# Performance work log

Hardware: AMD Instinct MI355X
Metric: run time of the kernel (lower is better)

Reference implementation:

```python
import jax, jax.numpy as jnp
import numpy as np
jax.config.update("jax_enable_x64", True)

N = 16384   # nodes
C = 16      # initial color vocabulary size
B = 64      # number of graphs in the batch
_rs = np.random.RandomState(42)
_MULTS = jnp.asarray((_rs.randint(1, 2 ** 62, size=C + 1).astype(np.int64) << 1) | 1)  # odd 64-bit hash multipliers


def setup_inputs() -> dict:
    key = jax.random.key(0)
    k1, k2, k3 = jax.random.split(key, 3)
    x = jax.random.randint(k1, (N,), 0, C, dtype=jnp.int64)
    adj_t = jax.random.randint(k2, (N, N), 0, 2).astype(jnp.float32)  # dense binary adjacency
    batch = jnp.sort(jax.random.randint(k3, (N,), 0, B, dtype=jnp.int64))
    return {"x": x, "adj_t": adj_t, "batch": batch}


def _wl_colors(x, adj_t):
    # One WL refinement step. The torch code hashes (own_color, sorted neighbor colors)
    # and assigns new ids by insertion order into an OrderedDict ('isolate' -> 0).
    # A sorted tuple of neighbor colors is equivalent to the neighbor color multiset,
    # which we represent as a count histogram and hash with a 64-bit wraparound
    # polynomial hash; ids are then assigned by first-occurrence (node-index) order.
    n = x.shape[0]
    onehot = jax.nn.one_hot(x, C, dtype=adj_t.dtype)                 # [N, C]
    nbr_hist = jnp.round(adj_t @ onehot).astype(jnp.int64)           # [N, C] neighbor color counts
    iso = (adj_t.sum(axis=1) + adj_t.sum(axis=0)) == 0               # isolated nodes
    h = x * _MULTS[0] + (nbr_hist * _MULTS[1:]).sum(axis=-1)         # int64 wraparound hash
    h = jnp.where(iso, jnp.int64(-(2 ** 63)), h)
    order = jnp.argsort(h)
    hs = h[order]
    new_grp = jnp.concatenate([jnp.ones((1,), bool), hs[1:] != hs[:-1]])
    gid = jnp.zeros(n, jnp.int64).at[order].set(jnp.cumsum(new_grp) - 1)   # group id per node
    first_of_grp = jax.ops.segment_min(jnp.arange(n), gid, num_segments=n)
    firsts = first_of_grp[gid]                                       # first node index with same signature
    is_first = (~iso) & (firsts == jnp.arange(n))
    rank = jnp.cumsum(is_first.astype(jnp.int64))                    # hashmap insertion order (1-based)
    return jnp.where(iso, 0, rank[firsts])                           # 'isolate' -> 0


def _histogram(colors, batch):
    # Per-graph color histogram; width padded to N+1 (max possible distinct colors)
    # for static shapes -- extra columns are zero and do not affect the L2 norm.
    num_colors = N + 1
    idx = batch * num_colors + colors
    out = jnp.zeros(B * num_colors, jnp.int64).at[idx].add(1)
    out = out.reshape(B, num_colors)[:, 1:]                          # drop 'isolate' column
    out = out.astype(jnp.float64)
    return out / jnp.linalg.norm(out, axis=-1, keepdims=True)


def reference(x, adj_t, batch):
    colors = _wl_colors(x, adj_t)          # forward's default return value
    hist = _histogram(colors, batch)       # return_embedding=True output
    return hist, colors
```

## Files before the change

### kernel.cpp

```cpp
#include <hip/hip_runtime.h>
#include <stdint.h>

#define NN 16384
#define NC 16
#define NB 64

typedef unsigned int vuint4 __attribute__((ext_vector_type(4)));

struct Mults { unsigned long long m[17]; };


__global__ __launch_bounds__(256) void k_init(const int* __restrict__ x,
                                              unsigned long long* __restrict__ table,
                                              int* __restrict__ scount,
                                              int* __restrict__ cnt) {
  int idx = blockIdx.x * 256 + threadIdx.x;
  if (idx == 0) *scount = 0;
  if (idx < 4096) {
    int c = idx & 15, k = (idx >> 4) & 3, chunk = idx >> 6;
    unsigned long long m = 0ull;
    for (int l = 0; l < 64; ++l) {
      int col = chunk * 256 + l * 4 + k;
      if (x[col] == c) m |= (1ull << l);
    }
    table[idx] = m;
  }
  int4 z = {0, 0, 0, 0};
  int4* c4 = (int4*)cnt;
  #pragma unroll
  for (int r = 0; r < 4; ++r) c4[(size_t)idx * 4 + r] = z;
}

__global__ __launch_bounds__(256) void k_hist(const float* __restrict__ adj,
                                              const unsigned long long* __restrict__ table,
                                              const int* __restrict__ x,
                                              Mults M,
                                              unsigned long long* __restrict__ h,
                                              int* __restrict__ iso,
                                              int* __restrict__ firsts,
                                              int* __restrict__ suspects,
                                              int* __restrict__ scount) {
  int wave = threadIdx.x >> 6;
  int lane = threadIdx.x & 63;
  int row  = blockIdx.x * 4 + wave;
  int xv   = x[row];
  const vuint4* rowp = (const vuint4*)(adj + (size_t)row * NN);
  int c = lane & 15, k = lane >> 6 ? 0 : (lane >> 4);
  k = lane >> 4;
  const unsigned long long* tk = table + (k * 16 + c);
  int cnt = 0;
  #pragma unroll 4
  for (int chunk = 0; chunk < 64; ++chunk) {
    vuint4 v = __builtin_nontemporal_load(&rowp[chunk * 64 + lane]);
    unsigned long long tm = tk[chunk * 64];
    unsigned long long b0 = __ballot(v.x != 0u);
    unsigned long long b1 = __ballot(v.y != 0u);
    unsigned long long b2 = __ballot(v.z != 0u);
    unsigned long long b3 = __ballot(v.w != 0u);
    unsigned long long m = (k & 2) ? ((k & 1) ? b3 : b2) : ((k & 1) ? b1 : b0);
    cnt += __popcll(m & tm);
  }
  cnt += __shfl_xor(cnt, 16, 64);
  cnt += __shfl_xor(cnt, 32, 64);
  int rs = cnt;
  rs += __shfl_xor(rs, 1, 64);
  rs += __shfl_xor(rs, 2, 64);
  rs += __shfl_xor(rs, 4, 64);
  rs += __shfl_xor(rs, 8, 64);
  unsigned long long hl = (unsigned long long)(long long)cnt * M.m[(lane & 15) + 1];
  hl += __shfl_xor(hl, 1, 64);
  hl += __shfl_xor(hl, 2, 64);
  hl += __shfl_xor(hl, 4, 64);
  hl += __shfl_xor(hl, 8, 64);
  if (lane == 0) {
    h[row] = hl + (unsigned long long)(long long)xv * M.m[0];
    if (rs == 0) { int s = atomicAdd(scount, 1); suspects[s] = row; }
  }
  if (lane == 1) iso[row] = 0;
  if (lane == 2) firsts[row] = 0x7fffffff;
}

__global__ __launch_bounds__(256) void k_colcheck(const float* __restrict__ adj,
                                                  const int* __restrict__ suspects,
                                                  const int* __restrict__ scount,
                                                  int* __restrict__ iso,
                                                  unsigned long long* __restrict__ h) {
  __shared__ int red[256];
  int nsus = *scount;
  for (int u = blockIdx.x; u < nsus; u += gridDim.x) {
    int col = suspects[u];
    int any = 0;
    for (int r = threadIdx.x; r < NN; r += 256)
      any |= (adj[(size_t)r * NN + col] != 0.0f);
    red[threadIdx.x] = any;
    __syncthreads();
    for (int s = 128; s > 0; s >>= 1) {
      if (threadIdx.x < s) red[threadIdx.x] |= red[threadIdx.x + s];
      __syncthreads();
    }
    if (threadIdx.x == 0 && red[0] == 0) {
      iso[col] = 1;
      h[col] = 0x8000000000000000ull;
    }
    __syncthreads();
  }
}

#define JC 2048
__global__ __launch_bounds__(256) void k_firsts(const unsigned long long* __restrict__ h,
                                                int* __restrict__ firsts) {
  __shared__ unsigned long long hs[JC];
  int jbase = blockIdx.y * JC;
  for (int t = threadIdx.x; t < JC; t += 256) hs[t] = h[jbase + t];
  __syncthreads();
  int i = blockIdx.x * 256 + threadIdx.x;
  unsigned long long hi = h[i];
  int best = 0x7fffffff;
  #pragma unroll 8
  for (int jj = 0; jj < JC; ++jj) {
    if (hs[jj] == hi) best = min(best, jbase + jj);
  }
  if (best < 0x7fffffff) atomicMin(&firsts[i], best);
}

__global__ __launch_bounds__(1024) void k_scan(const int* __restrict__ iso,
                                               const int* __restrict__ firsts,
                                               const int* __restrict__ batch,
                                               float* __restrict__ out_colors,
                                               int* __restrict__ cnt) {
  __shared__ int rank_lds[NN];
  __shared__ int wsum[16];
  int t = threadIdx.x;
  int lane = t & 63, wv = t >> 6;
  int base = t * 16;
  int loc[16];
  int s = 0;
  #pragma unroll
  for (int u = 0; u < 16; ++u) {
    int i = base + u;
    int isf = (!iso[i]) && (firsts[i] == i);
    s += isf;
    loc[u] = s;
  }
  int incl = s;
  #pragma unroll
  for (int off = 1; off < 64; off <<= 1) {
    int v = __shfl_up(incl, off, 64);
    if (lane >= off) incl += v;
  }
  if (lane == 63) wsum[wv] = incl;
  __syncthreads();
  if (t == 0) {
    int acc = 0;
    #pragma unroll
    for (int w = 0; w < 16; ++w) { int v = wsum[w]; wsum[w] = acc; acc += v; }
  }
  __syncthreads();
  int excl = wsum[wv] + incl - s;
  #pragma unroll
  for (int u = 0; u < 16; ++u) rank_lds[base + u] = excl + loc[u];
  __syncthreads();
  #pragma unroll
  for (int u = 0; u < 16; ++u) {
    int i = base + u;
    int c = iso[i] ? 0 : rank_lds[firsts[i]];
    out_colors[i] = (float)c;
    if (c > 0) atomicAdd(&cnt[(size_t)batch[i] * NN + (c - 1)], 1);
  }
}

__global__ __launch_bounds__(256) void k_norm(const int* __restrict__ cnt,
                                              float* __restrict__ out) {
  __shared__ float red[256];
  int b = blockIdx.x;
  const int4* c4 = (const int4*)(cnt + (size_t)b * NN);
  float4* o4 = (float4*)(out + (size_t)b * NN);
  float ss = 0.0f;
  for (int j = threadIdx.x; j < NN / 4; j += 256) {
    int4 v = c4[j];
    float4 f = {(float)v.x, (float)v.y, (float)v.z, (float)v.w};
    ss += f.x * f.x + f.y * f.y + f.z * f.z + f.w * f.w;
  }
  red[threadIdx.x] = ss;
  __syncthreads();
  for (int s = 128; s > 0; s >>= 1) {
    if (threadIdx.x < s) red[threadIdx.x] += red[threadIdx.x + s];
    __syncthreads();
  }
  float inv = 1.0f / sqrtf(red[0]);
  for (int j = threadIdx.x; j < NN / 4; j += 256) {
    int4 v = c4[j];
    float4 f = {(float)v.x * inv, (float)v.y * inv, (float)v.z * inv, (float)v.w * inv};
    o4[j] = f;
  }
}


struct MTState { uint32_t mt[624]; int idx; };

static void mt_seed(MTState& s, uint32_t seed) {
  s.mt[0] = seed;
  for (int i = 1; i < 624; ++i)
    s.mt[i] = 1812433253u * (s.mt[i - 1] ^ (s.mt[i - 1] >> 30)) + (uint32_t)i;
  s.idx = 624;
}

static uint32_t mt_next(MTState& s) {
  if (s.idx >= 624) {
    for (int i = 0; i < 624; ++i) {
      uint32_t y = (s.mt[i] & 0x80000000u) | (s.mt[(i + 1) % 624] & 0x7fffffffu);
      uint32_t nx = s.mt[(i + 397) % 624] ^ (y >> 1);
      if (y & 1u) nx ^= 2567483615u;
      s.mt[i] = nx;
    }
    s.idx = 0;
  }
  uint32_t y = s.mt[s.idx++];
  y ^= y >> 11;
  y ^= (y << 7) & 2636928640u;
  y ^= (y << 15) & 4022730752u;
  y ^= y >> 18;
  return y;
}

static uint64_t mt_next64(MTState& s) {
  uint64_t hi = mt_next(s);
  uint64_t lo = mt_next(s);
  return (hi << 32) | lo;
}


extern "C" void kernel_launch(void* const* d_in, const int* in_sizes, int n_in,
                              void* d_out, int out_size, void* d_ws, size_t ws_size,
                              hipStream_t stream) {
  const int*   x     = (const int*)d_in[0];
  const float* adj   = (const float*)d_in[1];
  const int*   batch = (const int*)d_in[2];
  float* out_hist   = (float*)d_out;
  float* out_colors = out_hist + (size_t)NB * NN;

  char* ws = (char*)d_ws;
  int*                cnt      = (int*)(ws + 0);
  int*                scount   = (int*)(ws + 4194304);
  int*                suspects = (int*)(ws + 4194560);
  unsigned long long* h        = (unsigned long long*)(ws + 4260096);
  int*                iso      = (int*)(ws + 4391168);
  int*                firsts   = (int*)(ws + 4456704);
  unsigned long long* table    = (unsigned long long*)(ws + 4522240);

  Mults M;
  {
    MTState st;
    mt_seed(st, 42u);
    const uint64_t mask62 = (1ull << 62) - 1ull;
    const uint64_t rng    = (1ull << 62) - 2ull;
    for (int i = 0; i < 17; ++i) {
      uint64_t v;
      do { v = mt_next64(st) & mask62; } while (v > rng);
      M.m[i] = ((1ull + v) << 1) | 1ull;
    }
  }

  k_init<<<256, 256, 0, stream>>>(x, table, scount, cnt);
  k_hist<<<NN / 4, 256, 0, stream>>>(adj, table, x, M, h, iso, firsts, suspects, scount);
  k_colcheck<<<64, 256, 0, stream>>>(adj, suspects, scount, iso, h);
  dim3 gf(NN / 256, NN / JC);
  k_firsts<<<gf, 256, 0, stream>>>(h, firsts);
  k_scan<<<1, 1024, 0, stream>>>(iso, firsts, batch, out_colors, cnt);
  k_norm<<<NB, 256, 0, stream>>>(cnt, out_hist);
}
```

Measured before the change: 1.409 ms.

## Replace O(N^2) first-occurrence search with global atomic hash table

Drops the all-pairs k_firsts kernel that compared every node's hash against every other node's. Non-isolated nodes now insert their hash into a 65536-slot open-addressing table using CAS, with atomicMin keeping the smallest node index per key. The scan kernel looks each node's key up in the table to find its first occurrence. This removes a quadratic compare pass, but adds atomic contention and serial probing in the single-block scan. The k_hist kernel, which streams the 1 GiB adjacency matrix, still dominates the runtime.

Measured after the change: 1.428 ms. About the same (+1.4%).

```diff
diff --git a/kernel.cpp b/kernel.cpp
--- a/kernel.cpp
+++ b/kernel.cpp
@@ -5,15 +5,34 @@
 #define NC 16
 #define NB 64
 
+#define HSIZE 65536
+#define HMASK 65535
+#define HSENT 0xFFFFFFFFFFFFFFFFull
+#define HGOLD 0x9E3779B97F4A7C15ull
+
 typedef unsigned int vuint4 __attribute__((ext_vector_type(4)));
 
 struct Mults { unsigned long long m[17]; };
+
+__device__ __forceinline__ void htab_insert(unsigned long long* __restrict__ hk,
+                                            int* __restrict__ hv,
+                                            unsigned long long key, int idx) {
+  if (key == HSENT) key -= 1;
+  unsigned slot = (unsigned)((key * HGOLD) >> 48);
+  for (;;) {
+    unsigned long long old = atomicCAS(&hk[slot], HSENT, key);
+    if (old == HSENT || old == key) { atomicMin(&hv[slot], idx); return; }
+    slot = (slot + 1) & HMASK;
+  }
+}
 
 
 __global__ __launch_bounds__(256) void k_init(const int* __restrict__ x,
                                               unsigned long long* __restrict__ table,
                                               int* __restrict__ scount,
-                                              int* __restrict__ cnt) {
+                                              int* __restrict__ cnt,
+                                              unsigned long long* __restrict__ hk,
+                                              int* __restrict__ hv) {
   int idx = blockIdx.x * 256 + threadIdx.x;
   if (idx == 0) *scount = 0;
   if (idx < 4096) {
@@ -25,6 +44,8 @@
     }
     table[idx] = m;
   }
+  hk[idx] = HSENT;
+  hv[idx] = 0x7fffffff;
   int4 z = {0, 0, 0, 0};
   int4* c4 = (int4*)cnt;
   #pragma unroll
@@ -37,16 +58,17 @@
                                               Mults M,
                                               unsigned long long* __restrict__ h,
                                               int* __restrict__ iso,
-                                              int* __restrict__ firsts,
                                               int* __restrict__ suspects,
-                                              int* __restrict__ scount) {
+                                              int* __restrict__ scount,
+                                              unsigned long long* __restrict__ hk,
+                                              int* __restrict__ hv) {
   int wave = threadIdx.x >> 6;
   int lane = threadIdx.x & 63;
   int row  = blockIdx.x * 4 + wave;
   int xv   = x[row];
   const vuint4* rowp = (const vuint4*)(adj + (size_t)row * NN);
-  int c = lane & 15, k = lane >> 6 ? 0 : (lane >> 4);
-  k = lane >> 4;
+  int c = lane & 15;
+  int k = lane >> 4;
   const unsigned long long* tk = table + (k * 16 + c);
   int cnt = 0;
   #pragma unroll 4
@@ -73,18 +95,25 @@
   hl += __shfl_xor(hl, 4, 64);
   hl += __shfl_xor(hl, 8, 64);
   if (lane == 0) {
-    h[row] = hl + (unsigned long long)(long long)xv * M.m[0];
-    if (rs == 0) { int s = atomicAdd(scount, 1); suspects[s] = row; }
+    unsigned long long hf = hl + (unsigned long long)(long long)xv * M.m[0];
+    h[row] = hf;
+    if (rs == 0) {
+      int s = atomicAdd(scount, 1);
+      suspects[s] = row;
+    } else {
+      htab_insert(hk, hv, hf, row);
+    }
   }
   if (lane == 1) iso[row] = 0;
-  if (lane == 2) firsts[row] = 0x7fffffff;
 }
 
 __global__ __launch_bounds__(256) void k_colcheck(const float* __restrict__ adj,
                                                   const int* __restrict__ suspects,
                                                   const int* __restrict__ scount,
                                                   int* __restrict__ iso,
-                                                  unsigned long long* __restrict__ h) {
+                                                  const unsigned long long* __restrict__ h,
+                                                  unsigned long long* __restrict__ hk,
+                                                  int* __restrict__ hv) {
   __shared__ int red[256];
   int nsus = *scount;
   for (int u = blockIdx.x; u < nsus; u += gridDim.x) {
@@ -98,33 +127,18 @@
       if (threadIdx.x < s) red[threadIdx.x] |= red[threadIdx.x + s];
       __syncthreads();
     }
-    if (threadIdx.x == 0 && red[0] == 0) {
-      iso[col] = 1;
-      h[col] = 0x8000000000000000ull;
+    if (threadIdx.x == 0) {
+      if (red[0] == 0) iso[col] = 1;
+      else             htab_insert(hk, hv, h[col], col);
     }
     __syncthreads();
   }
 }
 
-#define JC 2048
-__global__ __launch_bounds__(256) void k_firsts(const unsigned long long* __restrict__ h,
-                                                int* __restrict__ firsts) {
-  __shared__ unsigned long long hs[JC];
-  int jbase = blockIdx.y * JC;
-  for (int t = threadIdx.x; t < JC; t += 256) hs[t] = h[jbase + t];
-  __syncthreads();
-  int i = blockIdx.x * 256 + threadIdx.x;
-  unsigned long long hi = h[i];
-  int best = 0x7fffffff;
-  #pragma unroll 8
-  for (int jj = 0; jj < JC; ++jj) {
-    if (hs[jj] == hi) best = min(best, jbase + jj);
-  }
-  if (best < 0x7fffffff) atomicMin(&firsts[i], best);
-}
-
 __global__ __launch_bounds__(1024) void k_scan(const int* __restrict__ iso,
-                                               const int* __restrict__ firsts,
+                                               const unsigned long long* __restrict__ h,
+                                               const unsigned long long* __restrict__ hk,
+                                               const int* __restrict__ hv,
                                                const int* __restrict__ batch,
                                                float* __restrict__ out_colors,
                                                int* __restrict__ cnt) {
@@ -133,12 +147,23 @@
   int t = threadIdx.x;
   int lane = t & 63, wv = t >> 6;
   int base = t * 16;
+  int fidx[16];
   int loc[16];
   int s = 0;
   #pragma unroll
   for (int u = 0; u < 16; ++u) {
     int i = base + u;
-    int isf = (!iso[i]) && (firsts[i] == i);
+    int f = -1;
+    if (!iso[i]) {
+      unsigned long long key = h[i];
+      if (key == HSENT) key -= 1;
+      unsigned slot = (unsigned)((key * HGOLD) >> 48);
+      unsigned long long kk = hk[slot];
+      while (kk != key) { slot = (slot + 1) & HMASK; kk = hk[slot]; }
+      f = hv[slot];
+    }
+    fidx[u] = f;
+    int isf = (f == i);
     s += isf;
     loc[u] = s;
   }
@@ -163,7 +188,7 @@
   #pragma unroll
   for (int u = 0; u < 16; ++u) {
     int i = base + u;
-    int c = iso[i] ? 0 : rank_lds[firsts[i]];
+    int c = (fidx[u] < 0) ? 0 : rank_lds[fidx[u]];
     out_colors[i] = (float)c;
     if (c > 0) atomicAdd(&cnt[(size_t)batch[i] * NN + (c - 1)], 1);
   }
@@ -245,8 +270,9 @@
   int*                suspects = (int*)(ws + 4194560);
   unsigned long long* h        = (unsigned long long*)(ws + 4260096);
   int*                iso      = (int*)(ws + 4391168);
-  int*                firsts   = (int*)(ws + 4456704);
-  unsigned long long* table    = (unsigned long long*)(ws + 4522240);
+  unsigned long long* table    = (unsigned long long*)(ws + 4456704);
+  unsigned long long* hk       = (unsigned long long*)(ws + 4489216);
+  int*                hv       = (int*)(ws + 5013504);
 
   Mults M;
   {
@@ -261,11 +287,9 @@
     }
   }
 
-  k_init<<<256, 256, 0, stream>>>(x, table, scount, cnt);
-  k_hist<<<NN / 4, 256, 0, stream>>>(adj, table, x, M, h, iso, firsts, suspects, scount);
-  k_colcheck<<<64, 256, 0, stream>>>(adj, suspects, scount, iso, h);
-  dim3 gf(NN / 256, NN / JC);
-  k_firsts<<<gf, 256, 0, stream>>>(h, firsts);
-  k_scan<<<1, 1024, 0, stream>>>(iso, firsts, batch, out_colors, cnt);
+  k_init<<<256, 256, 0, stream>>>(x, table, scount, cnt, hk, hv);
+  k_hist<<<NN / 4, 256, 0, stream>>>(adj, table, x, M, h, iso, suspects, scount, hk, hv);
+  k_colcheck<<<64, 256, 0, stream>>>(adj, suspects, scount, iso, h, hk, hv);
+  k_scan<<<1, 1024, 0, stream>>>(iso, h, hk, hv, batch, out_colors, cnt);
   k_norm<<<NB, 256, 0, stream>>>(cnt, out_hist);
 }
```
